# Kernel tuning notes

Hardware: AMD Instinct MI355X
Metric: run time of the kernel (lower is better)

Reference implementation:

```python
import jax, jax.numpy as jnp
import numpy as np

EPS = 1e-6
HEADS = 8
DIM_HEAD = 64
SCALE = 16.0
DIM = 1024
INNER = HEADS * DIM_HEAD


def _l2norm(t):
    return t / jnp.clip(jnp.linalg.norm(t, axis=-1, keepdims=True), 1e-12)


def setup_inputs() -> dict:
    key = jax.random.key(0)
    k1, k2, k3, k4 = jax.random.split(key, 4)
    b, n = 2, 4096
    x = jax.random.normal(k1, (b, n, DIM), dtype=jnp.float32)
    # weights stored as [in, out] so application is x @ W
    Wq = jax.random.normal(k2, (DIM, INNER), dtype=jnp.float32) * 0.02
    Wkv = jax.random.normal(k3, (DIM, 2 * INNER), dtype=jnp.float32) * 0.02
    Wo = jax.random.normal(k4, (INNER, DIM), dtype=jnp.float32) * 0.02
    return {"x": x, "Wq": Wq, "Wkv": Wkv, "Wo": Wo}


def reference(x, Wq, Wkv, Wo):
    b, n, _ = x.shape
    q = (x @ Wq).reshape(b, n, HEADS, DIM_HEAD).transpose(0, 2, 1, 3)  # b h n d
    kv = x @ Wkv
    k = kv[..., :INNER].reshape(b, n, HEADS, DIM_HEAD).transpose(0, 2, 1, 3)
    v = kv[..., INNER:].reshape(b, n, HEADS, DIM_HEAD).transpose(0, 2, 1, 3)
    q = _l2norm(q)
    k = _l2norm(k)
    # cosine-sim attention: logits = scale * (q.k) - scale, logits <= 0 so exp is stable
    logits = jnp.einsum('bhid,bhjd->bhij', q, k) * SCALE - SCALE
    p = jnp.exp(logits)
    row_sums = jnp.clip(p.sum(axis=-1, keepdims=True), EPS)  # matches per-block EPS clamp in dense case
    out = jnp.einsum('bhij,bhjd->bhid', p, v) / row_sums  # b h n d
    out = out.transpose(0, 2, 1, 3).reshape(b, n, INNER)
    return out @ Wo
```

## Files before the change

kernel.cpp:

```cpp
#include <hip/hip_runtime.h>


typedef _Float16 f16;
typedef _Float16 f16x4 __attribute__((ext_vector_type(4)));
typedef _Float16 f16x8 __attribute__((ext_vector_type(8)));
typedef float f32x4 __attribute__((ext_vector_type(4)));
typedef float f32x16 __attribute__((ext_vector_type(16)));
typedef int i32x4 __attribute__((ext_vector_type(4)));

#define MFMA_F16(a, b, c) __builtin_amdgcn_mfma_f32_16x16x32_f16((a), (b), (c), 0, 0, 0)
#define MFMA32(a, b, c) __builtin_amdgcn_mfma_f32_32x32x16_f16((a), (b), (c), 0, 0, 0)

#define QSCALE 23.083120654223414f
#define EXPBIAS -9.083120654223414f

__device__ __forceinline__ void gl_lds16(const void* g, void* l) {
  __builtin_amdgcn_global_load_lds(
      (const __attribute__((address_space(1))) void*)g,
      (__attribute__((address_space(3))) void*)l, 16, 0, 0);
}

__global__ void convert_x_kernel(const float* __restrict__ x, f16* __restrict__ xh, int n8) {
  int i = blockIdx.x * 256 + threadIdx.x;
  if (i >= n8) return;
  const float4* xv = (const float4*)x;
  float4 a = xv[2 * i], b = xv[2 * i + 1];
  f16x8 o;
  o[0] = (f16)a.x; o[1] = (f16)a.y; o[2] = (f16)a.z; o[3] = (f16)a.w;
  o[4] = (f16)b.x; o[5] = (f16)b.y; o[6] = (f16)b.z; o[7] = (f16)b.w;
  ((f16x8*)xh)[i] = o;
}

__global__ void transpose_all_kernel(const float* __restrict__ Wq,
                                     const float* __restrict__ Wkv,
                                     const float* __restrict__ Wo,
                                     f16* __restrict__ Wqkv_t, f16* __restrict__ Wo_t) {
  __shared__ float t[64][65];
  const int z = blockIdx.z;
  const float* W; int ldw, col0, K, nc; f16* out;
  if (z == 0)      { W = Wq;  ldw = 512;  col0 = 0;   K = 1024; nc = 8;  out = Wqkv_t; }
  else if (z == 1) { W = Wkv; ldw = 1024; col0 = 0;   K = 1024; nc = 8;  out = Wqkv_t + 512 * 1024; }
  else if (z == 2) { W = Wkv; ldw = 1024; col0 = 512; K = 1024; nc = 8;  out = Wqkv_t + 1024 * 1024; }
  else             { W = Wo;  ldw = 1024; col0 = 0;   K = 512;  nc = 16; out = Wo_t; }
  if ((int)blockIdx.x >= nc || (int)blockIdx.y >= (K >> 6)) return;
  int tx = threadIdx.x, ty = threadIdx.y;
  int c0 = blockIdx.x * 64, k0 = blockIdx.y * 64;
#pragma unroll
  for (int i = 0; i < 8; i++)
    t[ty + i * 8][tx] = W[(long)(k0 + ty + i * 8) * ldw + col0 + c0 + tx];
  __syncthreads();
#pragma unroll
  for (int i = 0; i < 8; i++)
    out[(long)(c0 + ty + i * 8) * K + k0 + tx] = (f16)t[tx][ty + i * 8];
}

__global__ void transpose_v_kernel(const f16* __restrict__ Vb, f16* __restrict__ Vt, int n) {
  __shared__ f16 t[64 * 64];
  const int tid = threadIdx.x;
  const int bh = blockIdx.y;
  const int n0 = blockIdx.x * 64;
  const f16* src = Vb + ((long)bh * n + n0) * 64;
  const int j = tid >> 3, c = tid & 7;
  f16x8 v0 = *(const f16x8*)(src + j * 64 + c * 8);
  f16x8 v1 = *(const f16x8*)(src + (j + 32) * 64 + c * 8);
  *(f16x8*)(&t[j * 64 + ((c ^ (j & 7)) << 3)]) = v0;
  *(f16x8*)(&t[(j + 32) * 64 + ((c ^ (j & 7)) << 3)]) = v1;
  __syncthreads();
  const int d = tid >> 3, cj = tid & 7;
  f16x8 o0, o1;
#pragma unroll
  for (int e = 0; e < 8; e++) {
    int jj = cj * 8 + e;
    o0[e] = t[jj * 64 + (((d >> 3) ^ (jj & 7)) << 3) + (d & 7)];
    o1[e] = t[jj * 64 + ((((d + 32) >> 3) ^ (jj & 7)) << 3) + ((d + 32) & 7)];
  }
  *(f16x8*)(Vt + ((long)bh * 64 + d) * n + n0 + cj * 8) = o0;
  *(f16x8*)(Vt + ((long)bh * 64 + d + 32) * n + n0 + cj * 8) = o1;
}

template <int MODE>
__global__ __launch_bounds__(256, 3)
void gemm_kernel(const f16* __restrict__ A, const f16* __restrict__ Bt,
                 float* __restrict__ C,
                 f16* __restrict__ Qb, f16* __restrict__ Kb, f16* __restrict__ Vb,
                 int M, int N, int K) {
  __shared__ f16 As[128 * 32];
  __shared__ f16 Bs[128 * 32];
  const int tid = threadIdx.x;
  const int lane = tid & 63;
  const int wid = tid >> 6;
  const int wr = wid >> 1, wc = wid & 1;
  const int lr = lane & 15, lk = lane >> 4;
  const int lin = blockIdx.x;
  const int bx = ((lin & 7) << 3) | ((lin >> 3) & 7);
  const int by = lin >> 6;
  const long m0 = (long)bx * 128;
  const int n0 = by * 128;

  f32x4 acc[4][4] = {};

  const int c0 = tid, c1 = tid + 256;
  const int ar0 = c0 >> 2, ah0 = (c0 & 3) ^ ((ar0 >> 1) & 3);
  const int ar1 = c1 >> 2, ah1 = (c1 & 3) ^ ((ar1 >> 1) & 3);
  const f16* pa0 = A + (m0 + ar0) * K + ah0 * 8;
  const f16* pa1 = A + (m0 + ar1) * K + ah1 * 8;
  const f16* pb0 = Bt + (long)(n0 + ar0) * K + ah0 * 8;
  const f16* pb1 = Bt + (long)(n0 + ar1) * K + ah1 * 8;

  for (int k0 = 0; k0 < K; k0 += 32) {
    __syncthreads();
    gl_lds16(pa0 + k0, As + c0 * 8);
    gl_lds16(pa1 + k0, As + c1 * 8);
    gl_lds16(pb0 + k0, Bs + c0 * 8);
    gl_lds16(pb1 + k0, Bs + c1 * 8);
    __syncthreads();

    f16x8 af[4], bf[4];
#pragma unroll
    for (int mi = 0; mi < 4; mi++) {
      int row = wr * 64 + mi * 16 + lr;
      int ch = lk ^ ((row >> 1) & 3);
      af[mi] = *(const f16x8*)(As + row * 32 + ch * 8);
    }
#pragma unroll
    for (int ni = 0; ni < 4; ni++) {
      int row = wc * 64 + ni * 16 + lr;
      int ch = lk ^ ((row >> 1) & 3);
      bf[ni] = *(const f16x8*)(Bs + row * 32 + ch * 8);
    }
    __builtin_amdgcn_s_setprio(1);
#pragma unroll
    for (int mi = 0; mi < 4; mi++)
#pragma unroll
      for (int ni = 0; ni < 4; ni++)
        acc[mi][ni] = MFMA_F16(af[mi], bf[ni], acc[mi][ni]);
    __builtin_amdgcn_s_setprio(0);
  }

  if (MODE == 0) {
#pragma unroll
    for (int mi = 0; mi < 4; mi++) {
      long mrow = m0 + wr * 64 + mi * 16 + lk * 4;
#pragma unroll
      for (int r = 0; r < 4; r++)
#pragma unroll
        for (int ni = 0; ni < 4; ni++)
          C[(mrow + r) * N + n0 + wc * 64 + ni * 16 + lr] = acc[mi][ni][r];
    }
  } else {
    const int region = by >> 2;
    const int head = (by & 3) * 2 + wc;
    f16* buf = (region == 0) ? Qb : ((region == 1) ? Kb : Vb);
    const float nscale = (region == 0) ? QSCALE : 1.f;
#pragma unroll
    for (int mi = 0; mi < 4; mi++) {
      float scl[4];
      if (region < 2) {
#pragma unroll
        for (int r = 0; r < 4; r++) {
          float s2 = 0.f;
#pragma unroll
          for (int ni = 0; ni < 4; ni++) s2 += acc[mi][ni][r] * acc[mi][ni][r];
          s2 += __shfl_xor(s2, 1);
          s2 += __shfl_xor(s2, 2);
          s2 += __shfl_xor(s2, 4);
          s2 += __shfl_xor(s2, 8);
          scl[r] = nscale / fmaxf(sqrtf(s2), 1e-12f);
        }
      } else {
#pragma unroll
        for (int r = 0; r < 4; r++) scl[r] = 1.f;
      }
#pragma unroll
      for (int r = 0; r < 4; r++) {
        int m = (int)m0 + wr * 64 + mi * 16 + lk * 4 + r;
        int bb = m >> 12, nn = m & 4095;
        f16* dst = buf + (((long)(bb * 8 + head) * 4096 + nn) << 6);
#pragma unroll
        for (int ni = 0; ni < 4; ni++)
          dst[ni * 16 + lr] = (f16)(acc[mi][ni][r] * scl[r]);
      }
    }
  }
}

__global__ __launch_bounds__(256, 3)
void attn_kernel(const f16* __restrict__ Qb, const f16* __restrict__ Kb,
                 const f16* __restrict__ Vt, f16* __restrict__ Ob, int n) {
  __shared__ f16 Ks[2][128 * 64];
  __shared__ f16 Vs[64 * 128];
  const int tid = threadIdx.x, lane = tid & 63, wid = tid >> 6;
  const int ql = lane & 31, hi = lane >> 5;
  const int lin = blockIdx.x;
  const int bh = (lin & 7) | ((lin >> 8) << 3);
  const int qx = (lin >> 3) & 31;
  const long nl = n;
  const f16* Qg = Qb + (long)bh * nl * 64;
  const f16* Kg = Kb + (long)bh * nl * 64;
  const f16* Vg = Vt + (long)bh * 64 * nl;
  const int q0w = qx * 128 + wid * 32;

  f16x8 qf[4];
#pragma unroll
  for (int kc = 0; kc < 4; kc++)
    qf[kc] = *(const f16x8*)(Qg + (long)(q0w + ql) * 64 + kc * 16 + hi * 8);

  int ksrc[4], vsrc[4];
#pragma unroll
  for (int p = 0; p < 4; p++) {
    const int ci = tid + p * 256;
    const int kj = ci >> 3, kc_ = ci & 7;
    ksrc[p] = kj * 64 + ((kc_ ^ (kj & 7)) << 3);
    const int vd = ci >> 4, vc = ci & 15;
    vsrc[p] = vd * n + ((vc ^ (vd & 15)) << 3);
  }

  f32x16 oacc[2][2] = {};
  float rsum0 = 0.f, rsum1 = 0.f;
  f32x16 initv;
#pragma unroll
  for (int e = 0; e < 16; e++) initv[e] = EXPBIAS;
  const auto one2 = __builtin_amdgcn_cvt_pkrtz(1.f, 1.f);

#pragma unroll
  for (int p = 0; p < 4; p++)
    gl_lds16(Kg + ksrc[p], &Ks[0][(tid + p * 256) * 8]);
  __syncthreads();

  const int nt = n >> 7;
  for (int t = 0; t < nt; t++) {
    const int cur = t & 1;
    if (t + 1 < nt) {
      const long kadv = (long)(t + 1) * 8192;
#pragma unroll
      for (int p = 0; p < 4; p++)
        gl_lds16(Kg + kadv + ksrc[p], &Ks[cur ^ 1][(tid + p * 256) * 8]);
    }
    {
      const long vadv = (long)t * 128;
#pragma unroll
      for (int p = 0; p < 4; p++)
        gl_lds16(Vg + vadv + vsrc[p], &Vs[(tid + p * 256) * 8]);
    }

    f16x8 pf[8];
#pragma unroll
    for (int jt = 0; jt < 4; jt++) {
      const int j = jt * 32 + ql, sw = j & 7;
      __builtin_amdgcn_s_setprio(1);
      const f16x8 k0 = *(const f16x8*)(&Ks[cur][j * 64 + ((hi ^ sw) << 3)]);
      f32x16 s = MFMA32(k0, qf[0], initv);
#pragma unroll
      for (int kc = 1; kc < 4; kc++) {
        const f16x8 kf = *(const f16x8*)(&Ks[cur][j * 64 + ((((kc << 1) | hi) ^ sw) << 3)]);
        s = MFMA32(kf, qf[kc], s);
      }
      __builtin_amdgcn_s_setprio(0);

      int w[8];
#pragma unroll
      for (int m = 0; m < 8; m++) {
        const float pa = __builtin_amdgcn_exp2f(s[2 * m]);
        const float pb = __builtin_amdgcn_exp2f(s[2 * m + 1]);
        const auto h = __builtin_amdgcn_cvt_pkrtz(pa, pb);
        if (m & 1)
          rsum1 = __builtin_amdgcn_fdot2(h, one2, rsum1, false);
        else
          rsum0 = __builtin_amdgcn_fdot2(h, one2, rsum0, false);
        w[m] = __builtin_bit_cast(int, h);
      }
#pragma unroll
      for (int kl = 0; kl < 2; kl++) {
        int a0 = w[4 * kl + 0], a1 = w[4 * kl + 1];
        int a2 = w[4 * kl + 2], a3 = w[4 * kl + 3];
        asm volatile("v_permlane32_swap_b32 %0, %1" : "+v"(a0), "+v"(a2));
        asm volatile("v_permlane32_swap_b32 %0, %1" : "+v"(a1), "+v"(a3));
        i32x4 fi = {a0, a1, a2, a3};
        pf[jt * 2 + kl] = __builtin_bit_cast(f16x8, fi);
      }
    }

    __syncthreads();

    __builtin_amdgcn_s_setprio(1);
#pragma unroll
    for (int kb = 0; kb < 8; kb++) {
#pragma unroll
      for (int dt = 0; dt < 2; dt++) {
        const int d = dt * 32 + ql;
        const f16x8 vf =
            *(const f16x8*)(&Vs[d * 128 + ((((kb << 1) | hi) ^ (d & 15)) << 3)]);
        oacc[kb & 1][dt] = MFMA32(pf[kb], vf, oacc[kb & 1][dt]);
      }
    }
    __builtin_amdgcn_s_setprio(0);

    __syncthreads();
  }

  float rsum = rsum0 + rsum1;
  rsum += __shfl_xor(rsum, 32);
  const int bb = bh >> 3, hh = bh & 7;
#pragma unroll
  for (int r = 0; r < 16; r++) {
    const int qloc = (r & 3) + 8 * (r >> 2) + 4 * hi;
    const float sm = __shfl(rsum, qloc);
    const float inv = 1.f / fmaxf(sm, 0.016384f);
    f16* dst = Ob + (((long)(bb * 4096 + q0w + qloc)) << 9) + hh * 64;
    dst[ql] = (f16)((oacc[0][0][r] + oacc[1][0][r]) * inv);
    dst[32 + ql] = (f16)((oacc[0][1][r] + oacc[1][1][r]) * inv);
  }
}

extern "C" void kernel_launch(void* const* d_in, const int* in_sizes, int n_in,
                              void* d_out, int out_size, void* d_ws, size_t ws_size,
                              hipStream_t stream) {
  const float* x   = (const float*)d_in[0];
  const float* Wq  = (const float*)d_in[1];
  const float* Wkv = (const float*)d_in[2];
  const float* Wo  = (const float*)d_in[3];
  float* out = (float*)d_out;

  char* ws = (char*)d_ws;
  f16* xh     = (f16*)(ws);
  f16* Wqkv_t = (f16*)(ws + 16777216);
  f16* Wo_t   = (f16*)(ws + 19922944);
  f16* Qb     = (f16*)(ws + 20971520);
  f16* Kb     = (f16*)(ws + 29360128);
  f16* Vb     = (f16*)(ws + 37748736);
  f16* At     = (f16*)(ws + 46137344);
  f16* Vt     = xh;

  convert_x_kernel<<<4096, 256, 0, stream>>>(x, xh, 1048576);

  transpose_all_kernel<<<dim3(16, 16, 4), dim3(64, 8), 0, stream>>>(Wq, Wkv, Wo, Wqkv_t, Wo_t);

  gemm_kernel<1><<<768, 256, 0, stream>>>(xh, Wqkv_t, nullptr, Qb, Kb, Vb,
                                          8192, 1536, 1024);
  transpose_v_kernel<<<dim3(64, 16), 256, 0, stream>>>(Vb, Vt, 4096);
  attn_kernel<<<512, 256, 0, stream>>>(Qb, Kb, Vt, At, 4096);
  gemm_kernel<0><<<512, 256, 0, stream>>>(At, Wo_t, out, nullptr, nullptr, nullptr,
                                          8192, 1024, 512);
}
```

Measured before the change: 164.1 us.

## Split KV tile across two wave groups and double-buffer V in attention

The attention block grows to 512 threads. Two groups of four waves share the same 32-row query tiles and each processes half of every 128-key tile. At the end, partial output accumulators and row sums are combined through LDS. V is now double-buffered alongside K, which removes the mid-iteration barrier so V loads can overlap compute. The aim is more waves per CU and less sync stall, at the cost of extra LDS (64KB per block), a final cross-wave reduction, and changed occupancy bounds.

```diff
diff --git a/kernel.cpp b/kernel.cpp
--- a/kernel.cpp
+++ b/kernel.cpp
@@ -184,12 +184,13 @@
   }
 }
 
-__global__ __launch_bounds__(256, 3)
+__global__ __launch_bounds__(512, 4)
 void attn_kernel(const f16* __restrict__ Qb, const f16* __restrict__ Kb,
                  const f16* __restrict__ Vt, f16* __restrict__ Ob, int n) {
   __shared__ f16 Ks[2][128 * 64];
-  __shared__ f16 Vs[64 * 128];
+  __shared__ f16 Vs[2][64 * 128];
   const int tid = threadIdx.x, lane = tid & 63, wid = tid >> 6;
+  const int wq = wid & 3, wj = wid >> 2;
   const int ql = lane & 31, hi = lane >> 5;
   const int lin = blockIdx.x;
   const int bh = (lin & 7) | ((lin >> 8) << 3);
@@ -198,24 +199,24 @@
   const f16* Qg = Qb + (long)bh * nl * 64;
   const f16* Kg = Kb + (long)bh * nl * 64;
   const f16* Vg = Vt + (long)bh * 64 * nl;
-  const int q0w = qx * 128 + wid * 32;
+  const int q0w = qx * 128 + wq * 32;
 
   f16x8 qf[4];
 #pragma unroll
   for (int kc = 0; kc < 4; kc++)
     qf[kc] = *(const f16x8*)(Qg + (long)(q0w + ql) * 64 + kc * 16 + hi * 8);
 
-  int ksrc[4], vsrc[4];
-#pragma unroll
-  for (int p = 0; p < 4; p++) {
-    const int ci = tid + p * 256;
+  int ksrc[2], vsrc[2];
+#pragma unroll
+  for (int p = 0; p < 2; p++) {
+    const int ci = tid + p * 512;
     const int kj = ci >> 3, kc_ = ci & 7;
     ksrc[p] = kj * 64 + ((kc_ ^ (kj & 7)) << 3);
     const int vd = ci >> 4, vc = ci & 15;
     vsrc[p] = vd * n + ((vc ^ (vd & 15)) << 3);
   }
 
-  f32x16 oacc[2][2] = {};
+  f32x16 oacc[2] = {};
   float rsum0 = 0.f, rsum1 = 0.f;
   f32x16 initv;
 #pragma unroll
@@ -223,8 +224,10 @@
   const auto one2 = __builtin_amdgcn_cvt_pkrtz(1.f, 1.f);
 
 #pragma unroll
-  for (int p = 0; p < 4; p++)
-    gl_lds16(Kg + ksrc[p], &Ks[0][(tid + p * 256) * 8]);
+  for (int p = 0; p < 2; p++) {
+    gl_lds16(Kg + ksrc[p], &Ks[0][(tid + p * 512) * 8]);
+    gl_lds16(Vg + vsrc[p], &Vs[0][(tid + p * 512) * 8]);
+  }
   __syncthreads();
 
   const int nt = n >> 7;
@@ -232,21 +235,18 @@
     const int cur = t & 1;
     if (t + 1 < nt) {
       const long kadv = (long)(t + 1) * 8192;
-#pragma unroll
-      for (int p = 0; p < 4; p++)
-        gl_lds16(Kg + kadv + ksrc[p], &Ks[cur ^ 1][(tid + p * 256) * 8]);
-    }
-    {
-      const long vadv = (long)t * 128;
-#pragma unroll
-      for (int p = 0; p < 4; p++)
-        gl_lds16(Vg + vadv + vsrc[p], &Vs[(tid + p * 256) * 8]);
-    }
-
-    f16x8 pf[8];
-#pragma unroll
-    for (int jt = 0; jt < 4; jt++) {
-      const int j = jt * 32 + ql, sw = j & 7;
+      const long vadv = (long)(t + 1) * 128;
+#pragma unroll
+      for (int p = 0; p < 2; p++) {
+        gl_lds16(Kg + kadv + ksrc[p], &Ks[cur ^ 1][(tid + p * 512) * 8]);
+        gl_lds16(Vg + vadv + vsrc[p], &Vs[cur ^ 1][(tid + p * 512) * 8]);
+      }
+    }
+
+    f16x8 pf[4];
+#pragma unroll
+    for (int jt = 0; jt < 2; jt++) {
+      const int j = wj * 64 + jt * 32 + ql, sw = j & 7;
       __builtin_amdgcn_s_setprio(1);
       const f16x8 k0 = *(const f16x8*)(&Ks[cur][j * 64 + ((hi ^ sw) << 3)]);
       f32x16 s = MFMA32(k0, qf[0], initv);
@@ -280,17 +280,16 @@
       }
     }
 
-    __syncthreads();
-
     __builtin_amdgcn_s_setprio(1);
 #pragma unroll
-    for (int kb = 0; kb < 8; kb++) {
+    for (int kbl = 0; kbl < 4; kbl++) {
+      const int kb = wj * 4 + kbl;
 #pragma unroll
       for (int dt = 0; dt < 2; dt++) {
         const int d = dt * 32 + ql;
         const f16x8 vf =
-            *(const f16x8*)(&Vs[d * 128 + ((((kb << 1) | hi) ^ (d & 15)) << 3)]);
-        oacc[kb & 1][dt] = MFMA32(pf[kb], vf, oacc[kb & 1][dt]);
+            *(const f16x8*)(&Vs[cur][d * 128 + ((((kb << 1) | hi) ^ (d & 15)) << 3)]);
+        oacc[dt] = MFMA32(pf[kbl], vf, oacc[dt]);
       }
     }
     __builtin_amdgcn_s_setprio(0);
@@ -300,15 +299,32 @@
 
   float rsum = rsum0 + rsum1;
   rsum += __shfl_xor(rsum, 32);
-  const int bb = bh >> 3, hh = bh & 7;
-#pragma unroll
-  for (int r = 0; r < 16; r++) {
-    const int qloc = (r & 3) + 8 * (r >> 2) + 4 * hi;
-    const float sm = __shfl(rsum, qloc);
-    const float inv = 1.f / fmaxf(sm, 0.016384f);
-    f16* dst = Ob + (((long)(bb * 4096 + q0w + qloc)) << 9) + hh * 64;
-    dst[ql] = (f16)((oacc[0][0][r] + oacc[1][0][r]) * inv);
-    dst[32 + ql] = (f16)((oacc[0][1][r] + oacc[1][1][r]) * inv);
+
+  float* red = (float*)&Ks[0][0];
+  float* redsum = (float*)&Vs[0][0];
+  if (wj == 1) {
+    f32x16* dst = (f32x16*)red + (wq * 64 + lane) * 2;
+    dst[0] = oacc[0];
+    dst[1] = oacc[1];
+    redsum[wq * 64 + lane] = rsum;
+  }
+  __syncthreads();
+  if (wj == 0) {
+    f32x16* srcp = (f32x16*)red + (wq * 64 + lane) * 2;
+    oacc[0] += srcp[0];
+    oacc[1] += srcp[1];
+    rsum += redsum[wq * 64 + lane];
+
+    const int bb = bh >> 3, hh = bh & 7;
+#pragma unroll
+    for (int r = 0; r < 16; r++) {
+      const int qloc = (r & 3) + 8 * (r >> 2) + 4 * hi;
+      const float sm = __shfl(rsum, qloc);
+      const float inv = 1.f / fmaxf(sm, 0.016384f);
+      f16* dst = Ob + (((long)(bb * 4096 + q0w + qloc)) << 9) + hh * 64;
+      dst[ql] = (f16)(oacc[0][r] * inv);
+      dst[32 + ql] = (f16)(oacc[1][r] * inv);
+    }
   }
 }
 
@@ -338,7 +354,7 @@
   gemm_kernel<1><<<768, 256, 0, stream>>>(xh, Wqkv_t, nullptr, Qb, Kb, Vb,
                                           8192, 1536, 1024);
   transpose_v_kernel<<<dim3(64, 16), 256, 0, stream>>>(Vb, Vt, 4096);
-  attn_kernel<<<512, 256, 0, stream>>>(Qb, Kb, Vt, At, 4096);
+  attn_kernel<<<512, 512, 0, stream>>>(Qb, Kb, Vt, At, 4096);
   gemm_kernel<0><<<512, 256, 0, stream>>>(At, Wo_t, out, nullptr, nullptr, nullptr,
                                           8192, 1024, 512);
 }
```

New measurement: 160.6 us. 1.02x faster.
